# Kernel optimization log

Hardware: AMD Instinct MI355X
Metric: run time of the kernel (lower is better)

## Reference

```python
import jax, jax.numpy as jnp
import numpy as np

EMBED_DIM = 768
NUM_HEADS = 12
HEAD_DIM = EMBED_DIM // NUM_HEADS


def setup_inputs() -> dict:
    key = jax.random.key(0)
    ks = jax.random.split(key, 9)
    B, S, D = 8, 1024, EMBED_DIM
    s = 1.0 / np.sqrt(D)
    return {
        "x": jax.random.normal(ks[0], (B, S, D), jnp.float32),
        "wq": jax.random.normal(ks[1], (D, D), jnp.float32) * s,
        "bq": jnp.zeros((D,), jnp.float32),
        "wk": jax.random.normal(ks[2], (D, D), jnp.float32) * s,
        "bk": jnp.zeros((D,), jnp.float32),
        "wv": jax.random.normal(ks[3], (D, D), jnp.float32) * s,
        "bv": jnp.zeros((D,), jnp.float32),
        "wo": jax.random.normal(ks[4], (D, D), jnp.float32) * s,
        "bo": jnp.zeros((D,), jnp.float32),
    }


def reference(x, wq, bq, wk, bk, wv, bv, wo, bo):
    B, S, D = x.shape
    H, Hd = NUM_HEADS, HEAD_DIM
    # QKV projections, reshape to [B, H, S, Hd]
    def proj(w, b):
        return (x @ w + b).reshape(B, S, H, Hd).transpose(0, 2, 1, 3)
    q = proj(wq, bq)
    k = proj(wk, bk)
    v = proj(wv, bv)
    # scaled dot-product attention (full matrix, as in source)
    scores = jnp.einsum('bhqd,bhkd->bhqk', q, k) / jnp.sqrt(jnp.float32(Hd))
    attn_w = jax.nn.softmax(scores, axis=-1)  # dropout p=0 -> identity
    attn = jnp.einsum('bhqk,bhkd->bhqd', attn_w, v)
    attn = attn.transpose(0, 2, 1, 3).reshape(B, S, D)
    return attn @ wo + bo
```

## Files before the change

kernel.cpp:

```cpp
#include <hip/hip_runtime.h>
#include <stdint.h>


#define AS_GLOBAL __attribute__((address_space(1)))
#define AS_LDS    __attribute__((address_space(3)))

typedef __attribute__((ext_vector_type(4))) float f32x4;
typedef __attribute__((ext_vector_type(8))) short bf16x8;
typedef unsigned short u16;
typedef unsigned int   u32;

#define L2E 1.44269504088896340736f

__device__ __forceinline__ u16 f2bf(float f) {
  u32 u = __float_as_uint(f);
  u += 0x7FFFu + ((u >> 16) & 1u);
  return (u16)(u >> 16);
}
__device__ __forceinline__ float bf2f(u16 h) {
  return __uint_as_float(((u32)h) << 16);
}
__device__ __forceinline__ void split2(float f, u16 &hi, u16 &lo) {
  hi = f2bf(f);
  lo = f2bf(f - bf2f(hi));
}
__device__ __forceinline__ void gl2lds16(const void* g, void* l) {
  __builtin_amdgcn_global_load_lds((const AS_GLOBAL u32*)g, (AS_LDS u32*)l, 16, 0, 0);
}
__device__ __forceinline__ int swz(int row, int kc) {
  return row * 64 + ((kc ^ (row & 7)) << 3);
}
__device__ __forceinline__ void mfma16(f32x4 &acc, bf16x8 a, bf16x8 b) {
  asm volatile("v_mfma_f32_16x16x32_bf16 %0, %1, %2, %0" : "+v"(acc) : "v"(a), "v"(b));
}

__global__ __launch_bounds__(256) void pack_x_kernel(
    const float* __restrict__ src, u16* __restrict__ dh, u16* __restrict__ dl, int n4) {
  int i = blockIdx.x * 256 + threadIdx.x;
  if (i >= n4) return;
  const float4 v = ((const float4*)src)[i];
  ushort4 h, lo;
  split2(v.x, h.x, lo.x); split2(v.y, h.y, lo.y);
  split2(v.z, h.z, lo.z); split2(v.w, h.w, lo.w);
  ((ushort4*)dh)[i] = h;  ((ushort4*)dl)[i] = lo;
}

__global__ __launch_bounds__(256) void pack_wT_kernel(
    const float* __restrict__ w, u16* __restrict__ dh, u16* __restrict__ dl, int K, int N) {
  int i = blockIdx.x * 256 + threadIdx.x;
  int n = i % N, k0 = (i / N) * 4;
  if (k0 >= K) return;
  ushort4 h, lo;
  split2(w[(size_t)(k0 + 0) * N + n], h.x, lo.x);
  split2(w[(size_t)(k0 + 1) * N + n], h.y, lo.y);
  split2(w[(size_t)(k0 + 2) * N + n], h.z, lo.z);
  split2(w[(size_t)(k0 + 3) * N + n], h.w, lo.w);
  *(ushort4*)&dh[(size_t)n * K + k0] = h;
  *(ushort4*)&dl[(size_t)n * K + k0] = lo;
}

template<int EPI>
__global__ __launch_bounds__(256) void gemm_split(
    const u16* __restrict__ Ahp, const u16* __restrict__ Alp,
    const u16* __restrict__ Bhp, const u16* __restrict__ Blp,
    int Ntx, int K0,
    const float* __restrict__ b0, const float* __restrict__ b1, const float* __restrict__ b2,
    u16* __restrict__ Qh, u16* __restrict__ Ql,
    u16* __restrict__ Kh, u16* __restrict__ Kl,
    u16* __restrict__ Vth, u16* __restrict__ Vtl,
    float* __restrict__ outF) {
  __shared__ u16 lA[128 * 64];
  __shared__ u16 lB[128 * 64];
  const int bid  = blockIdx.x;
  const int bcol = bid % Ntx;
  const int brow = bid / Ntx;
  const int t = threadIdx.x;
  const int l = t & 63, w = t >> 6;
  const int wm = w >> 1, wn = w & 1;
  const int l15 = l & 15, lg = l >> 4;

  f32x4 acc[4][4] = {};
  const int KP = K0 >> 6;

  for (int phase = 0; phase < 3; ++phase) {
    const u16* sA = (phase == 1) ? Alp : Ahp;
    const u16* sB = (phase == 2) ? Blp : Bhp;
    for (int ktp = 0; ktp < KP; ++ktp) {
      __syncthreads();
      #pragma unroll
      for (int it = 0; it < 4; ++it) {
        const int ci  = it * 256 + t;
        const int row = ci >> 3;
        const int gs  = (ci & 7) ^ (row & 7);
        gl2lds16(sA + (size_t)(brow * 128 + row) * K0 + ktp * 64 + gs * 8, &lA[ci * 8]);
        gl2lds16(sB + (size_t)(bcol * 128 + row) * K0 + ktp * 64 + gs * 8, &lB[ci * 8]);
      }
      __syncthreads();
      #pragma unroll
      for (int ks = 0; ks < 2; ++ks) {
        bf16x8 af[4], bfr[4];
        #pragma unroll
        for (int r = 0; r < 4; ++r)
          af[r] = *(const bf16x8*)&lA[swz(wm * 64 + r * 16 + l15, ks * 4 + lg)];
        #pragma unroll
        for (int c = 0; c < 4; ++c)
          bfr[c] = *(const bf16x8*)&lB[swz(wn * 64 + c * 16 + l15, ks * 4 + lg)];
        #pragma unroll
        for (int r = 0; r < 4; ++r)
          #pragma unroll
          for (int c = 0; c < 4; ++c)
            mfma16(acc[r][c], af[r], bfr[c]);
      }
    }
  }

  #pragma unroll
  for (int r = 0; r < 4; ++r) {
    #pragma unroll
    for (int c = 0; c < 4; ++c) {
      const int m0 = brow * 128 + wm * 64 + r * 16 + lg * 4;
      const int n  = bcol * 128 + wn * 64 + c * 16 + l15;
      if (EPI == 0) {
        const int which = n / 768;
        const int d  = n - which * 768;
        const float bias = (which == 0 ? b0 : which == 1 ? b1 : b2)[d];
        const int hh = d >> 6, hd = d & 63;
        const int b  = m0 >> 10, s0 = m0 & 1023;
        const size_t hb = ((size_t)(b * 12 + hh)) << 16;
        if (which == 0) {
          #pragma unroll
          for (int j = 0; j < 4; ++j) {
            u16 hi, lo; split2((acc[r][c][j] + bias) * 0.125f, hi, lo);
            const size_t a = hb + (size_t)(s0 + j) * 64 + hd;
            Qh[a] = hi; Ql[a] = lo;
          }
        } else if (which == 1) {
          #pragma unroll
          for (int j = 0; j < 4; ++j) {
            u16 hi, lo; split2(acc[r][c][j] + bias, hi, lo);
            const size_t a = hb + (size_t)(s0 + j) * 64 + hd;
            Kh[a] = hi; Kl[a] = lo;
          }
        } else {
          ushort4 h4, l4;
          split2(acc[r][c][0] + bias, h4.x, l4.x);
          split2(acc[r][c][1] + bias, h4.y, l4.y);
          split2(acc[r][c][2] + bias, h4.z, l4.z);
          split2(acc[r][c][3] + bias, h4.w, l4.w);
          const size_t a = hb + (size_t)hd * 1024 + s0;
          *(ushort4*)&Vth[a] = h4;
          *(ushort4*)&Vtl[a] = l4;
        }
      } else {
        const float bias = b0[n];
        #pragma unroll
        for (int j = 0; j < 4; ++j)
          outF[(size_t)(m0 + j) * 768 + n] = acc[r][c][j] + bias;
      }
    }
  }
}

__global__ __launch_bounds__(256) void attn_kernel(
    const u16* __restrict__ Qh, const u16* __restrict__ Ql,
    const u16* __restrict__ Kh, const u16* __restrict__ Kl,
    const u16* __restrict__ Vth, const u16* __restrict__ Vtl,
    u16* __restrict__ Oh, u16* __restrict__ Ol) {
  __shared__ u16 lK[2][64 * 64];
  __shared__ u16 lV[2][64 * 64];
  __shared__ u16 lP[2][64 * 72];
  const int bh = blockIdx.y, qt = blockIdx.x;
  const int t = threadIdx.x;
  const int l = t & 63, w = t >> 6;
  const int l15 = l & 15, lg = l >> 4;
  const size_t base = (size_t)bh << 16;

  bf16x8 qfh[2], qfl[2];
  {
    const size_t qr = base + (size_t)(qt * 64 + w * 16 + l15) * 64;
    #pragma unroll
    for (int ks = 0; ks < 2; ++ks) {
      qfh[ks] = *(const bf16x8*)&Qh[qr + ks * 32 + lg * 8];
      qfl[ks] = *(const bf16x8*)&Ql[qr + ks * 32 + lg * 8];
    }
  }
  float mrun[4], lrun[4];
  f32x4 Oacc[4] = {};
  #pragma unroll
  for (int j = 0; j < 4; ++j) { mrun[j] = -3.0e38f; lrun[j] = 0.f; }

  for (int kt = 0; kt < 16; ++kt) {
    __syncthreads();
    #pragma unroll
    for (int it = 0; it < 2; ++it) {
      const int ci  = it * 256 + t;
      const int row = ci >> 3;
      const int gs  = (ci & 7) ^ (row & 7);
      const size_t ka = base + (size_t)(kt * 64 + row) * 64 + gs * 8;
      gl2lds16(&Kh[ka],  &lK[0][ci * 8]);
      gl2lds16(&Kl[ka],  &lK[1][ci * 8]);
      const size_t va = base + (size_t)row * 1024 + kt * 64 + gs * 8;
      gl2lds16(&Vth[va], &lV[0][ci * 8]);
      gl2lds16(&Vtl[va], &lV[1][ci * 8]);
    }
    __syncthreads();

    f32x4 sc[4] = {};
    #pragma unroll
    for (int ks = 0; ks < 2; ++ks) {
      #pragma unroll
      for (int c = 0; c < 4; ++c) {
        const int idx = swz(c * 16 + l15, ks * 4 + lg);
        const bf16x8 kh = *(const bf16x8*)&lK[0][idx];
        const bf16x8 kl = *(const bf16x8*)&lK[1][idx];
        mfma16(sc[c], qfh[ks], kh);
        mfma16(sc[c], qfl[ks], kh);
        mfma16(sc[c], qfh[ks], kl);
      }
    }

    #pragma unroll
    for (int j = 0; j < 4; ++j) {
      float tm = fmaxf(fmaxf(sc[0][j], sc[1][j]), fmaxf(sc[2][j], sc[3][j]));
      #pragma unroll
      for (int d = 1; d < 16; d <<= 1) tm = fmaxf(tm, __shfl_xor(tm, d, 64));
      const float mnew  = fmaxf(mrun[j], tm);
      const float scale = exp2f((mrun[j] - mnew) * L2E);
      mrun[j] = mnew;
      float ps = 0.f;
      #pragma unroll
      for (int c = 0; c < 4; ++c) {
        const float pv = exp2f((sc[c][j] - mnew) * L2E);
        sc[c][j] = pv;
        ps += pv;
      }
      #pragma unroll
      for (int d = 1; d < 16; d <<= 1) ps += __shfl_xor(ps, d, 64);
      lrun[j] = lrun[j] * scale + ps;
      #pragma unroll
      for (int c2 = 0; c2 < 4; ++c2) Oacc[c2][j] *= scale;
    }

    #pragma unroll
    for (int c = 0; c < 4; ++c)
      #pragma unroll
      for (int j = 0; j < 4; ++j) {
        u16 hi, lo; split2(sc[c][j], hi, lo);
        const int pa = (w * 16 + lg * 4 + j) * 72 + c * 16 + l15;
        lP[0][pa] = hi; lP[1][pa] = lo;
      }

    #pragma unroll
    for (int ks = 0; ks < 2; ++ks) {
      const int pr = (w * 16 + l15) * 72 + ks * 32 + lg * 8;
      const bf16x8 ph = *(const bf16x8*)&lP[0][pr];
      const bf16x8 pl = *(const bf16x8*)&lP[1][pr];
      #pragma unroll
      for (int c2 = 0; c2 < 4; ++c2) {
        const int idx = swz(c2 * 16 + l15, ks * 4 + lg);
        const bf16x8 vh = *(const bf16x8*)&lV[0][idx];
        const bf16x8 vl = *(const bf16x8*)&lV[1][idx];
        mfma16(Oacc[c2], ph, vh);
        mfma16(Oacc[c2], pl, vh);
        mfma16(Oacc[c2], ph, vl);
      }
    }
  }

  const int b = bh / 12, hh = bh - b * 12;
  #pragma unroll
  for (int c2 = 0; c2 < 4; ++c2)
    #pragma unroll
    for (int j = 0; j < 4; ++j) {
      const float o = Oacc[c2][j] / lrun[j];
      const int q   = qt * 64 + w * 16 + lg * 4 + j;
      const int col = hh * 64 + c2 * 16 + l15;
      const size_t a = ((size_t)b * 1024 + q) * 768 + col;
      u16 hi, lo; split2(o, hi, lo);
      Oh[a] = hi; Ol[a] = lo;
    }
}

extern "C" void kernel_launch(void* const* d_in, const int* in_sizes, int n_in,
                              void* d_out, int out_size, void* d_ws, size_t ws_size,
                              hipStream_t stream) {
  const float* x  = (const float*)d_in[0];
  const float* wq = (const float*)d_in[1];
  const float* bq = (const float*)d_in[2];
  const float* wk = (const float*)d_in[3];
  const float* bk = (const float*)d_in[4];
  const float* wv = (const float*)d_in[5];
  const float* bv = (const float*)d_in[6];
  const float* wo = (const float*)d_in[7];
  const float* bo = (const float*)d_in[8];

  const int M = 8192, D = 768, BH = 96;
  char* p = (char*)d_ws;
  auto carve = [&](size_t bytes) -> char* {
    char* r = p; p += (bytes + 255) & ~(size_t)255; return r;
  };
  u16* xh     = (u16*)carve((size_t)M * D * 2);
  u16* xl     = (u16*)carve((size_t)M * D * 2);
  u16* wqkvTh = (u16*)carve((size_t)3 * D * D * 2);
  u16* wqkvTl = (u16*)carve((size_t)3 * D * D * 2);
  u16* woTh   = (u16*)carve((size_t)D * D * 2);
  u16* woTl   = (u16*)carve((size_t)D * D * 2);
  u16* Qh  = (u16*)carve((size_t)BH * 1024 * 64 * 2);
  u16* Ql  = (u16*)carve((size_t)BH * 1024 * 64 * 2);
  u16* Kh  = (u16*)carve((size_t)BH * 1024 * 64 * 2);
  u16* Kl  = (u16*)carve((size_t)BH * 1024 * 64 * 2);
  u16* Vth = (u16*)carve((size_t)BH * 1024 * 64 * 2);
  u16* Vtl = (u16*)carve((size_t)BH * 1024 * 64 * 2);
  u16* attnh = xh;
  u16* attnl = xl;

  pack_x_kernel<<<(M * D / 4 + 255) / 256, 256, 0, stream>>>(x, xh, xl, M * D / 4);
  const int wgrid = (D * (D / 4) + 255) / 256;
  pack_wT_kernel<<<wgrid, 256, 0, stream>>>(wq, wqkvTh + 0 * (size_t)D * D, wqkvTl + 0 * (size_t)D * D, D, D);
  pack_wT_kernel<<<wgrid, 256, 0, stream>>>(wk, wqkvTh + 1 * (size_t)D * D, wqkvTl + 1 * (size_t)D * D, D, D);
  pack_wT_kernel<<<wgrid, 256, 0, stream>>>(wv, wqkvTh + 2 * (size_t)D * D, wqkvTl + 2 * (size_t)D * D, D, D);
  pack_wT_kernel<<<wgrid, 256, 0, stream>>>(wo, woTh, woTl, D, D);

  gemm_split<0><<<(M / 128) * (2304 / 128), 256, 0, stream>>>(
      xh, xl, wqkvTh, wqkvTl, 2304 / 128, D,
      bq, bk, bv, Qh, Ql, Kh, Kl, Vth, Vtl, nullptr);

  attn_kernel<<<dim3(16, BH), 256, 0, stream>>>(Qh, Ql, Kh, Kl, Vth, Vtl, attnh, attnl);

  gemm_split<1><<<(M / 128) * (D / 128), 256, 0, stream>>>(
      attnh, attnl, woTh, woTl, D / 128, D,
      bo, nullptr, nullptr,
      nullptr, nullptr, nullptr, nullptr, nullptr, nullptr, (float*)d_out);
}
```

Measured before the change: 400.8 us.

## Prefetch next K/V tile into registers and remap attention blocks per XCD

```diff
diff --git a/kernel.cpp b/kernel.cpp
--- a/kernel.cpp
+++ b/kernel.cpp
@@ -161,7 +161,7 @@
   }
 }
 
-__global__ __launch_bounds__(256) void attn_kernel(
+__global__ __launch_bounds__(256, 3) void attn_kernel(
     const u16* __restrict__ Qh, const u16* __restrict__ Ql,
     const u16* __restrict__ Kh, const u16* __restrict__ Kl,
     const u16* __restrict__ Vth, const u16* __restrict__ Vtl,
@@ -169,11 +169,51 @@
   __shared__ u16 lK[2][64 * 64];
   __shared__ u16 lV[2][64 * 64];
   __shared__ u16 lP[2][64 * 72];
-  const int bh = blockIdx.y, qt = blockIdx.x;
+
+  const int bid = blockIdx.x;
+  const int xcd = bid & 7, kk = bid >> 3;
+  const int bh  = xcd * 12 + (kk >> 4);
+  const int qt  = kk & 15;
+
   const int t = threadIdx.x;
   const int l = t & 63, w = t >> 6;
   const int l15 = l & 15, lg = l >> 4;
   const size_t base = (size_t)bh << 16;
+
+  bf16x8 stg[2][4];
+  const int ci0 = t, row0 = ci0 >> 3, c80 = ci0 & 7;
+  const int ci1 = t + 256, row1 = ci1 >> 3, c81 = ci1 & 7;
+  const int dst0 = row0 * 64 + ((c80 ^ (row0 & 7)) << 3);
+  const int dst1 = row1 * 64 + ((c81 ^ (row1 & 7)) << 3);
+
+  auto issue = [&](int kt) {
+    {
+      const size_t ka = base + (size_t)(kt * 64 + row0) * 64 + c80 * 8;
+      const size_t va = base + (size_t)row0 * 1024 + kt * 64 + c80 * 8;
+      stg[0][0] = *(const bf16x8*)&Kh[ka];
+      stg[0][1] = *(const bf16x8*)&Kl[ka];
+      stg[0][2] = *(const bf16x8*)&Vth[va];
+      stg[0][3] = *(const bf16x8*)&Vtl[va];
+    }
+    {
+      const size_t ka = base + (size_t)(kt * 64 + row1) * 64 + c81 * 8;
+      const size_t va = base + (size_t)row1 * 1024 + kt * 64 + c81 * 8;
+      stg[1][0] = *(const bf16x8*)&Kh[ka];
+      stg[1][1] = *(const bf16x8*)&Kl[ka];
+      stg[1][2] = *(const bf16x8*)&Vth[va];
+      stg[1][3] = *(const bf16x8*)&Vtl[va];
+    }
+  };
+  auto commit = [&]() {
+    *(bf16x8*)&lK[0][dst0] = stg[0][0];
+    *(bf16x8*)&lK[1][dst0] = stg[0][1];
+    *(bf16x8*)&lV[0][dst0] = stg[0][2];
+    *(bf16x8*)&lV[1][dst0] = stg[0][3];
+    *(bf16x8*)&lK[0][dst1] = stg[1][0];
+    *(bf16x8*)&lK[1][dst1] = stg[1][1];
+    *(bf16x8*)&lV[0][dst1] = stg[1][2];
+    *(bf16x8*)&lV[1][dst1] = stg[1][3];
+  };
 
   bf16x8 qfh[2], qfl[2];
   {
@@ -189,21 +229,12 @@
   #pragma unroll
   for (int j = 0; j < 4; ++j) { mrun[j] = -3.0e38f; lrun[j] = 0.f; }
 
+  issue(0);
+  commit();
+  __syncthreads();
+
   for (int kt = 0; kt < 16; ++kt) {
-    __syncthreads();
-    #pragma unroll
-    for (int it = 0; it < 2; ++it) {
-      const int ci  = it * 256 + t;
-      const int row = ci >> 3;
-      const int gs  = (ci & 7) ^ (row & 7);
-      const size_t ka = base + (size_t)(kt * 64 + row) * 64 + gs * 8;
-      gl2lds16(&Kh[ka],  &lK[0][ci * 8]);
-      gl2lds16(&Kl[ka],  &lK[1][ci * 8]);
-      const size_t va = base + (size_t)row * 1024 + kt * 64 + gs * 8;
-      gl2lds16(&Vth[va], &lV[0][ci * 8]);
-      gl2lds16(&Vtl[va], &lV[1][ci * 8]);
-    }
-    __syncthreads();
+    if (kt < 15) issue(kt + 1);
 
     f32x4 sc[4] = {};
     #pragma unroll
@@ -265,6 +296,10 @@
         mfma16(Oacc[c2], ph, vl);
       }
     }
+
+    __syncthreads();
+    if (kt < 15) commit();
+    __syncthreads();
   }
 
   const int b = bh / 12, hh = bh - b * 12;
@@ -325,7 +360,7 @@
       xh, xl, wqkvTh, wqkvTl, 2304 / 128, D,
       bq, bk, bv, Qh, Ql, Kh, Kl, Vth, Vtl, nullptr);
 
-  attn_kernel<<<dim3(16, BH), 256, 0, stream>>>(Qh, Ql, Kh, Kl, Vth, Vtl, attnh, attnl);
+  attn_kernel<<<16 * BH, 256, 0, stream>>>(Qh, Ql, Kh, Kl, Vth, Vtl, attnh, attnl);
 
   gemm_split<1><<<(M / 128) * (D / 128), 256, 0, stream>>>(
       attnh, attnl, woTh, woTl, D / 128, D,
```

After: 423.2 us. 5.6% more time.
